# Optimization experiments

Measured on AMD Instinct MI355X. Metric: run time of the kernel, lower is better.

The kernel has to match this reference:

```python
import jax, jax.numpy as jnp
import numpy as np

DT = 1.0 / 200.0  # imu_freq = 200
EPS = 1e-8

def _skew(v):  # [B,3] -> [B,3,3]
    x, y, z = v[:, 0], v[:, 1], v[:, 2]
    zero = jnp.zeros_like(x)
    return jnp.stack([zero, -z, y, z, zero, -x, -y, x, zero], axis=-1).reshape(-1, 3, 3)

def _axis_angle_to_R(w, dt):
    # Rodrigues: R = I + sin(th) K + (1-cos(th)) K^2, th = ||w||*dt
    n = jnp.linalg.norm(w, axis=-1, keepdims=True)          # [B,1]
    theta = n[:, 0] * dt                                     # [B]
    axis = w / (n + EPS)
    K = _skew(axis)
    I = jnp.eye(3, dtype=w.dtype)
    s = jnp.sin(theta)[:, None, None]
    c = jnp.cos(theta)[:, None, None]
    return I + s * K + (1.0 - c) * jnp.einsum('bij,bjk->bik', K, K)

def _R_to_axis_angle(R):
    tr = jnp.trace(R, axis1=-2, axis2=-1)
    angle = jnp.arccos(jnp.clip((tr - 1.0) / 2.0, -1.0 + 1e-7, 1.0 - 1e-7))
    axis = jnp.stack([R[:, 2, 1] - R[:, 1, 2],
                      R[:, 0, 2] - R[:, 2, 0],
                      R[:, 1, 0] - R[:, 0, 1]], axis=-1)
    axis = axis / (2.0 * jnp.sin(angle)[:, None] + EPS)
    return axis, angle

def _aa_to_quat(axis, angle):  # (w, x, y, z)
    h = angle / 2.0
    return jnp.concatenate([jnp.cos(h)[:, None], axis * jnp.sin(h)[:, None]], axis=-1)

def setup_inputs() -> dict:
    key = jax.random.key(0)
    input_seq = jax.random.normal(key, (512, 4096, 6), dtype=jnp.float32)
    return {"input_seq": input_seq}

def reference(input_seq):
    B, T, _ = input_seq.shape
    dtype = input_seq.dtype
    w = jnp.transpose(input_seq[:, :, :3], (1, 0, 2))  # [T,B,3] gyro
    a = jnp.transpose(input_seq[:, :, 3:], (1, 0, 2))  # [T,B,3] accel
    dt = jnp.asarray(DT, dtype)
    dt2_half = dt * dt / 2.0

    dR0 = jnp.broadcast_to(jnp.eye(3, dtype=dtype), (B, 3, 3))
    dv0 = jnp.zeros((B, 3), dtype)
    dp0 = jnp.zeros((B, 3), dtype)

    def step(carry, inp):
        dR, dv, dp = carry
        w_k, a_k = inp
        dR = jnp.einsum('bij,bjk->bik', dR, _axis_angle_to_R(w_k, dt))
        Ra = jnp.einsum('bij,bj->bi', dR, a_k)
        dv = dv + Ra * dt
        dp = dp + dv * dt + Ra * dt2_half  # uses already-updated dv, as in torch code
        axis, angle = _R_to_axis_angle(dR)
        q = _aa_to_quat(axis, angle)
        return (dR, dv, dp), (dp, dv, q)

    _, (ps, vs, qs) = jax.lax.scan(step, (dR0, dv0, dp0), (w, a))
    ps = jnp.transpose(ps, (1, 0, 2))  # [B,T,3]
    vs = jnp.transpose(vs, (1, 0, 2))  # [B,T,3]
    qs = jnp.transpose(qs, (1, 0, 2))  # [B,T,4]
    return jnp.concatenate([input_seq, ps, qs, vs], axis=2)  # [B,T,16]
```

## Files before the change

kernel.cpp:

```cpp
#include <hip/hip_runtime.h>
#include <math.h>

#define T_LEN 4096
#define CHUNK 16
#define NTHR  256
#define ESTRIDE 15

__device__ __forceinline__ void make_A(float wx, float wy, float wz, float* A) {
    const float dt = 1.0f / 200.0f;
    float n = sqrtf(wx*wx + wy*wy + wz*wz);
    float theta = n * dt;
    float inv = 1.0f / (n + 1e-8f);
    float x = wx * inv, y = wy * inv, z = wz * inv;
    float s = sinf(theta);
    float c = cosf(theta);
    float oc = 1.0f - c;
    A[0] = 1.0f + oc * (-(y*y + z*z));
    A[1] = -s*z + oc * (x*y);
    A[2] =  s*y + oc * (x*z);
    A[3] =  s*z + oc * (x*y);
    A[4] = 1.0f + oc * (-(x*x + z*z));
    A[5] = -s*x + oc * (y*z);
    A[6] = -s*y + oc * (x*z);
    A[7] =  s*x + oc * (y*z);
    A[8] = 1.0f + oc * (-(x*x + y*y));
}

__device__ __forceinline__ void matmul3(const float* R, const float* A, float* N) {
#pragma unroll
    for (int i = 0; i < 3; ++i) {
        N[i*3+0] = R[i*3+0]*A[0] + R[i*3+1]*A[3] + R[i*3+2]*A[6];
        N[i*3+1] = R[i*3+0]*A[1] + R[i*3+1]*A[4] + R[i*3+2]*A[7];
        N[i*3+2] = R[i*3+0]*A[2] + R[i*3+1]*A[5] + R[i*3+2]*A[8];
    }
}

__device__ __forceinline__ void step(float* R, float* v, float* p,
                                     float wx, float wy, float wz,
                                     float ax, float ay, float az) {
    const float dt   = 1.0f / 200.0f;
    const float dt2h = dt * dt * 0.5f;
    float A[9], N[9];
    make_A(wx, wy, wz, A);
    matmul3(R, A, N);
#pragma unroll
    for (int i = 0; i < 9; ++i) R[i] = N[i];
    float rax = R[0]*ax + R[1]*ay + R[2]*az;
    float ray = R[3]*ax + R[4]*ay + R[5]*az;
    float raz = R[6]*ax + R[7]*ay + R[8]*az;
    v[0] += rax*dt; v[1] += ray*dt; v[2] += raz*dt;
    p[0] += v[0]*dt + rax*dt2h;
    p[1] += v[1]*dt + ray*dt2h;
    p[2] += v[2]*dt + raz*dt2h;
}

__global__ __launch_bounds__(NTHR)
void preint_kernel(const float* __restrict__ in, float* __restrict__ out) {
    const int b = blockIdx.x;
    const int t = threadIdx.x;
    const float dt = 1.0f / 200.0f;

    const float* bin  = in  + (size_t)b * T_LEN * 6;
    float*       bout = out + (size_t)b * T_LEN * 16;
    const float2* cin2 = (const float2*)(bin + (size_t)t * CHUNK * 6);

    float R[9] = {1,0,0, 0,1,0, 0,0,1};
    float v[3] = {0,0,0};
    float p[3] = {0,0,0};
#pragma unroll 4
    for (int k = 0; k < CHUNK; ++k) {
        float2 u0 = cin2[k*3+0];
        float2 u1 = cin2[k*3+1];
        float2 u2 = cin2[k*3+2];
        step(R, v, p, u0.x, u0.y, u1.x, u1.y, u2.x, u2.y);
    }

    __shared__ float lds[NTHR * ESTRIDE];
    float* e = lds + t * ESTRIDE;
#pragma unroll
    for (int i = 0; i < 9; ++i) e[i] = R[i];
    e[9]  = v[0]; e[10] = v[1]; e[11] = v[2];
    e[12] = p[0]; e[13] = p[1]; e[14] = p[2];
    __syncthreads();

    for (int d = 1; d < NTHR; d <<= 1) {
        float L[15];
        const bool act = (t >= d);
        if (act) {
            const float* src = lds + (t - d) * ESTRIDE;
#pragma unroll
            for (int i = 0; i < 15; ++i) L[i] = src[i];
        }
        __syncthreads();
        if (act) {
            const float tau2 = (float)(d * CHUNK) * dt;
            float NA[9];
            matmul3(L, R, NA);
            float nb0 = L[9]  + L[0]*v[0] + L[1]*v[1] + L[2]*v[2];
            float nb1 = L[10] + L[3]*v[0] + L[4]*v[1] + L[5]*v[2];
            float nb2 = L[11] + L[6]*v[0] + L[7]*v[1] + L[8]*v[2];
            float nc0 = L[12] + tau2*L[9]  + L[0]*p[0] + L[1]*p[1] + L[2]*p[2];
            float nc1 = L[13] + tau2*L[10] + L[3]*p[0] + L[4]*p[1] + L[5]*p[2];
            float nc2 = L[14] + tau2*L[11] + L[6]*p[0] + L[7]*p[1] + L[8]*p[2];
#pragma unroll
            for (int i = 0; i < 9; ++i) R[i] = NA[i];
            v[0] = nb0; v[1] = nb1; v[2] = nb2;
            p[0] = nc0; p[1] = nc1; p[2] = nc2;
#pragma unroll
            for (int i = 0; i < 9; ++i) e[i] = R[i];
            e[9]  = v[0]; e[10] = v[1]; e[11] = v[2];
            e[12] = p[0]; e[13] = p[1]; e[14] = p[2];
        }
        __syncthreads();
    }

    float S[9]  = {1,0,0, 0,1,0, 0,0,1};
    float sv[3] = {0,0,0};
    float sp[3] = {0,0,0};
    if (t > 0) {
        const float* src = lds + (t - 1) * ESTRIDE;
#pragma unroll
        for (int i = 0; i < 9; ++i) S[i] = src[i];
        sv[0] = src[9];  sv[1] = src[10]; sv[2] = src[11];
        sp[0] = src[12]; sp[1] = src[13]; sp[2] = src[14];
    }

#pragma unroll 4
    for (int k = 0; k < CHUNK; ++k) {
        float2 u0 = cin2[k*3+0];
        float2 u1 = cin2[k*3+1];
        float2 u2 = cin2[k*3+2];
        step(S, sv, sp, u0.x, u0.y, u1.x, u1.y, u2.x, u2.y);

        float tr  = S[0] + S[4] + S[8];
        float ca  = fminf(fmaxf(0.5f * (tr - 1.0f), -1.0f + 1e-7f), 1.0f - 1e-7f);
        float ang = acosf(ca);
        float isc = 1.0f / (2.0f * sinf(ang) + 1e-8f);
        float axx = (S[7] - S[5]) * isc;
        float axy = (S[2] - S[6]) * isc;
        float axz = (S[3] - S[1]) * isc;
        float h   = 0.5f * ang;
        float qw  = cosf(h);
        float qs  = sinf(h);

        float4* orow = (float4*)(bout + (size_t)(t * CHUNK + k) * 16);
        orow[0] = make_float4(u0.x, u0.y, u1.x, u1.y);
        orow[1] = make_float4(u2.x, u2.y, sp[0], sp[1]);
        orow[2] = make_float4(sp[2], qw, axx * qs, axy * qs);
        orow[3] = make_float4(axz * qs, sv[0], sv[1], sv[2]);
    }
}

extern "C" void kernel_launch(void* const* d_in, const int* in_sizes, int n_in,
                              void* d_out, int out_size, void* d_ws, size_t ws_size,
                              hipStream_t stream) {
    const float* in = (const float*)d_in[0];
    float* out = (float*)d_out;
    const int B = in_sizes[0] / (T_LEN * 6);
    preint_kernel<<<dim3(B), dim3(NTHR), 0, stream>>>(in, out);
}
```

Baseline: 222.0 us.

## Double threads per sequence, cache inputs in registers, closed-form quaternion output

Halves the per-thread chunk and doubles threads per block, so the serial stepping work per thread shrinks while the block scan gains one more level. Each thread's inputs are loaded once into registers with float4 loads and reused in both passes instead of being re-read from global memory. The acos/sin/cos quaternion computation is replaced by the half-angle identity qw=sqrt((1+c)/2) with q_xyz = skew-difference/(4qw), which removes the transcendentals but changes numerics near angle=pi and drops the 1e-8 epsilon. Output rows are written in pairs as eight float4 stores.

Measured after the change: 207.3 us. -6.6%, faster.

```diff
diff --git a/kernel.cpp b/kernel.cpp
--- a/kernel.cpp
+++ b/kernel.cpp
@@ -2,8 +2,8 @@
 #include <math.h>
 
 #define T_LEN 4096
-#define CHUNK 16
-#define NTHR  256
+#define CHUNK 8
+#define NTHR  512
 #define ESTRIDE 15
 
 __device__ __forceinline__ void make_A(float wx, float wy, float wz, float* A) {
@@ -62,17 +62,25 @@
 
     const float* bin  = in  + (size_t)b * T_LEN * 6;
     float*       bout = out + (size_t)b * T_LEN * 16;
-    const float2* cin2 = (const float2*)(bin + (size_t)t * CHUNK * 6);
+
+    float in_reg[CHUNK * 6];
+    {
+        const float4* src4 = (const float4*)(bin + (size_t)t * CHUNK * 6);
+#pragma unroll
+        for (int i = 0; i < (CHUNK * 6) / 4; ++i) {
+            float4 u = src4[i];
+            in_reg[i*4+0] = u.x; in_reg[i*4+1] = u.y;
+            in_reg[i*4+2] = u.z; in_reg[i*4+3] = u.w;
+        }
+    }
 
     float R[9] = {1,0,0, 0,1,0, 0,0,1};
     float v[3] = {0,0,0};
     float p[3] = {0,0,0};
-#pragma unroll 4
+#pragma unroll
     for (int k = 0; k < CHUNK; ++k) {
-        float2 u0 = cin2[k*3+0];
-        float2 u1 = cin2[k*3+1];
-        float2 u2 = cin2[k*3+2];
-        step(R, v, p, u0.x, u0.y, u1.x, u1.y, u2.x, u2.y);
+        const float* u = in_reg + k * 6;
+        step(R, v, p, u[0], u[1], u[2], u[3], u[4], u[5]);
     }
 
     __shared__ float lds[NTHR * ESTRIDE];
@@ -125,29 +133,31 @@
         sp[0] = src[12]; sp[1] = src[13]; sp[2] = src[14];
     }
 
-#pragma unroll 4
-    for (int k = 0; k < CHUNK; ++k) {
-        float2 u0 = cin2[k*3+0];
-        float2 u1 = cin2[k*3+1];
-        float2 u2 = cin2[k*3+2];
-        step(S, sv, sp, u0.x, u0.y, u1.x, u1.y, u2.x, u2.y);
+#pragma unroll
+    for (int kk = 0; kk < CHUNK; kk += 2) {
+        float4 row[8];
+#pragma unroll
+        for (int j = 0; j < 2; ++j) {
+            const int k = kk + j;
+            const float* u = in_reg + k * 6;
+            step(S, sv, sp, u[0], u[1], u[2], u[3], u[4], u[5]);
 
-        float tr  = S[0] + S[4] + S[8];
-        float ca  = fminf(fmaxf(0.5f * (tr - 1.0f), -1.0f + 1e-7f), 1.0f - 1e-7f);
-        float ang = acosf(ca);
-        float isc = 1.0f / (2.0f * sinf(ang) + 1e-8f);
-        float axx = (S[7] - S[5]) * isc;
-        float axy = (S[2] - S[6]) * isc;
-        float axz = (S[3] - S[1]) * isc;
-        float h   = 0.5f * ang;
-        float qw  = cosf(h);
-        float qs  = sinf(h);
+            float tr  = S[0] + S[4] + S[8];
+            float ca  = fminf(fmaxf(0.5f * (tr - 1.0f), -1.0f + 1e-7f), 1.0f - 1e-7f);
+            float qw  = sqrtf(0.5f * (1.0f + ca));
+            float i4  = 0.25f / qw;
+            float qx  = (S[7] - S[5]) * i4;
+            float qy  = (S[2] - S[6]) * i4;
+            float qz  = (S[3] - S[1]) * i4;
 
-        float4* orow = (float4*)(bout + (size_t)(t * CHUNK + k) * 16);
-        orow[0] = make_float4(u0.x, u0.y, u1.x, u1.y);
-        orow[1] = make_float4(u2.x, u2.y, sp[0], sp[1]);
-        orow[2] = make_float4(sp[2], qw, axx * qs, axy * qs);
-        orow[3] = make_float4(axz * qs, sv[0], sv[1], sv[2]);
+            row[j*4+0] = make_float4(u[0], u[1], u[2], u[3]);
+            row[j*4+1] = make_float4(u[4], u[5], sp[0], sp[1]);
+            row[j*4+2] = make_float4(sp[2], qw, qx, qy);
+            row[j*4+3] = make_float4(qz, sv[0], sv[1], sv[2]);
+        }
+        float4* orow = (float4*)(bout + (size_t)(t * CHUNK + kk) * 16);
+#pragma unroll
+        for (int i = 0; i < 8; ++i) orow[i] = row[i];
     }
 }
 
```
